# Kernel tuning notes

Hardware: AMD Instinct MI355X
Metric: run time of the kernel (lower is better)

Reference implementation:

```python
import jax, jax.numpy as jnp
import numpy as np
import math

H = 8
E = 512
D_K = E // H
NEG = -1000000000.0
# last (and only surviving) row of dist_bar: one threshold per head
DIST_BAR = np.array([0.2, 0.3, 0.4, 0.5, 0.6, 0.7, 0.8, 0.9], dtype=np.float32)


def setup_inputs() -> dict:
    key = jax.random.key(0)
    ks = jax.random.split(key, 12)
    B, N = 8, 1024
    s = 1.0 / math.sqrt(E)
    inp = {
        "query": jax.random.normal(ks[0], (B, N, E), jnp.float32),
        "key": jax.random.normal(ks[1], (B, N, E), jnp.float32),
        "value": jax.random.normal(ks[2], (B, N, E), jnp.float32),
        "dist": jax.random.uniform(ks[3], (B, 1, N, N), jnp.float32),
        "mask": jnp.ones((B, N, N), jnp.int32),
        "Wq": jax.random.normal(ks[4], (E, E), jnp.float32) * s,
        "bq": jnp.zeros((E,), jnp.float32),
        "Wk": jax.random.normal(ks[5], (E, E), jnp.float32) * s,
        "bk": jnp.zeros((E,), jnp.float32),
        "Wv": jax.random.normal(ks[6], (E, E), jnp.float32) * s,
        "bv": jnp.zeros((E,), jnp.float32),
        "Wo": jax.random.normal(ks[7], (E, E), jnp.float32) * s,
        "bo": jnp.zeros((E,), jnp.float32),
    }
    return inp


def reference(query, key, value, dist, mask, Wq, bq, Wk, bk, Wv, bv, Wo, bo):
    B, N, _ = query.shape
    # project and split heads: [B, H, N, D_K]
    def heads(x, W, b):
        return (x @ W.T + b).reshape(B, N, H, D_K).transpose(0, 2, 1, 3)
    q = heads(query, Wq, bq)
    k = heads(key, Wk, bk)
    v = heads(value, Wv, bv)
    scores = jnp.einsum("bhqd,bhkd->bhqk", q, k) / math.sqrt(D_K)
    # padding mask: [B,N,N] -> [B,1,N,N]
    scores = jnp.where(mask[:, None, :, :] == 0, NEG, scores)
    # per-head distance mask: dist [B,1,N,N] < thr[h] -> [B,H,N,N]
    thr = jnp.asarray(DIST_BAR)[None, :, None, None]
    dmask = dist < thr
    # first row/col (global atom) always attend
    dmask = dmask.at[:, :, 0, :].set(True).at[:, :, :, 0].set(True)
    scores = jnp.where(dmask, scores, NEG)
    p = jax.nn.softmax(scores, axis=-1)
    out = jnp.einsum("bhqk,bhkd->bhqd", p, v)  # [B,H,N,D_K]
    out = out.transpose(0, 2, 1, 3).reshape(B, N, H * D_K)
    return out @ Wo.T + bo
```

## Files before the change

### kernel.cpp

```cpp
#include <hip/hip_runtime.h>
#include <stdint.h>


typedef __attribute__((ext_vector_type(8))) short short8;
typedef __attribute__((ext_vector_type(4))) float floatx4;

#define MFMA16(a, b, c) __builtin_amdgcn_mfma_f32_16x16x32_bf16((a), (b), (c), 0, 0, 0)

static __device__ __forceinline__ unsigned short f2bf(float f) {
  union { float f; unsigned u; } v; v.f = f;
  unsigned r = v.u + 0x7fffu + ((v.u >> 16) & 1u);
  return (unsigned short)(r >> 16);
}

static __device__ __forceinline__ void gload_lds16(const void* g, void* l) {
  __builtin_amdgcn_global_load_lds((const __attribute__((address_space(1))) unsigned int*)g,
                                   (__attribute__((address_space(3))) unsigned int*)l,
                                   16, 0, 0);
}
static __device__ __forceinline__ int xsw(int row) { return (row & 3) ^ ((row >> 2) & 3); }

__global__ void wcast_kernel(const float* __restrict__ Wq, const float* __restrict__ Wk,
                             const float* __restrict__ Wv, const float* __restrict__ Wo,
                             unsigned short* __restrict__ o0, unsigned short* __restrict__ o1,
                             unsigned short* __restrict__ o2, unsigned short* __restrict__ o3) {
  int i = blockIdx.x * blockDim.x + threadIdx.x;
  int w = i >> 16, loc = i & 65535;
  const float* s = (w == 0) ? Wq : (w == 1) ? Wk : (w == 2) ? Wv : Wo;
  unsigned short* d = (w == 0) ? o0 : (w == 1) ? o1 : (w == 2) ? o2 : o3;
  float4 v = ((const float4*)s)[loc];
  ushort4 o;
  o.x = f2bf(v.x); o.y = f2bf(v.y); o.z = f2bf(v.z); o.w = f2bf(v.w);
  ((ushort4*)d)[loc] = o;
}

__global__ void codes_kernel(const float* __restrict__ dist, const int* __restrict__ mask,
                             unsigned char* __restrict__ codesP) {
  int t = blockIdx.x * blockDim.x + threadIdx.x;
  int flat = t << 2;
  int b = flat >> 20;
  int rem = flat & ((1 << 20) - 1);
  int row = rem >> 10;
  int col0 = rem & 1023;
  float4 d4 = ((const float4*)dist)[t];
  int4 m4 = ((const int4*)mask)[t];
  float dv[4] = {d4.x, d4.y, d4.z, d4.w};
  int mv[4] = {m4.x, m4.y, m4.z, m4.w};
  int rg = row >> 5;
  int st = (row >> 4) & 1;
  int qq = (row >> 2) & 3;
  int r = row & 3;
  size_t rowbase = (size_t)(b * 32 + rg) * 32768;
  int sub = st * 32 + r;
#pragma unroll
  for (int u = 0; u < 4; u++) {
    int col = col0 + u;
    float d = dv[u];
    int hmin = (d >= 0.2f) + (d >= 0.3f) + (d >= 0.4f) + (d >= 0.5f) +
               (d >= 0.6f) + (d >= 0.7f) + (d >= 0.8f) + (d >= 0.9f);
    unsigned char cc = (unsigned char)hmin;
    if (row == 0 || col == 0) cc = 0;
    if (mv[u] == 0) cc = 9;
    int kt = col >> 7, ci = (col >> 4) & 7, c = col & 15;
    int lane = qq * 16 + c;
    codesP[rowbase + (size_t)kt * 4096 + lane * 64 + sub + ci * 4] = cc;
  }
}

__global__ __launch_bounds__(256) void qkv_gemm(
    const float* __restrict__ Aq, const float* __restrict__ Ak, const float* __restrict__ Av,
    const unsigned short* __restrict__ Wqp, const unsigned short* __restrict__ Wkp,
    const unsigned short* __restrict__ Wvp,
    const float* __restrict__ bq, const float* __restrict__ bk, const float* __restrict__ bv,
    unsigned short* __restrict__ Qh, unsigned short* __restrict__ Kh,
    unsigned short* __restrict__ Vt) {
  const int z = blockIdx.z;
  const float* A = (z == 0) ? Aq : (z == 1) ? Ak : Av;
  const unsigned short* W = (z == 0) ? Wqp : (z == 1) ? Wkp : Wvp;
  const float* bias = (z == 0) ? bq : (z == 1) ? bk : bv;
  unsigned short* O = (z == 0) ? Qh : (z == 1) ? Kh : Vt;

  __shared__ __align__(16) short As[64 * 40];
  __shared__ __align__(16) short Bs[128 * 32];
  const int tid = threadIdx.x;
  const int lane = tid & 63;
  const int wave = tid >> 6;
  const int c = lane & 15;
  const int q = lane >> 4;
  const int m0 = blockIdx.x * 64;
  const int n0 = blockIdx.y * 128;
  const int wr = (wave >> 1) * 32;
  const int wc = (wave & 1) * 64;

  floatx4 acc[2][4];
#pragma unroll
  for (int i = 0; i < 2; i++)
#pragma unroll
    for (int j = 0; j < 4; j++) acc[i][j] = (floatx4)(0.0f);

  const int arow = tid >> 2, ach = tid & 3;
  const float* Ab = A + (size_t)(m0 + arow) * 512 + ach * 8;

  for (int k0 = 0; k0 < 512; k0 += 32) {
    __syncthreads();
#pragma unroll
    for (int it = 0; it < 2; it++) {
      int slot = wave * 128 + it * 64 + lane;
      int brow = slot >> 2, bch = slot & 3;
      int g = bch ^ xsw(brow);
      gload_lds16(W + (size_t)(n0 + brow) * 512 + k0 + g * 8,
                  &Bs[(size_t)(wave * 128 + it * 64) * 8]);
    }
    float4 a0 = *(const float4*)(Ab + k0);
    float4 a1 = *(const float4*)(Ab + k0 + 4);
    short8 av;
    av[0] = (short)f2bf(a0.x); av[1] = (short)f2bf(a0.y);
    av[2] = (short)f2bf(a0.z); av[3] = (short)f2bf(a0.w);
    av[4] = (short)f2bf(a1.x); av[5] = (short)f2bf(a1.y);
    av[6] = (short)f2bf(a1.z); av[7] = (short)f2bf(a1.w);
    *(short8*)(&As[arow * 40 + ach * 8]) = av;
    __syncthreads();

    short8 af[2], bfv[4];
#pragma unroll
    for (int i = 0; i < 2; i++)
      af[i] = *(const short8*)(&As[(wr + i * 16 + c) * 40 + q * 8]);
#pragma unroll
    for (int j = 0; j < 4; j++) {
      int row = wc + j * 16 + c;
      bfv[j] = *(const short8*)(&Bs[row * 32 + (q ^ xsw(row)) * 8]);
    }
#pragma unroll
    for (int i = 0; i < 2; i++)
#pragma unroll
      for (int j = 0; j < 4; j++)
        acc[i][j] = MFMA16(af[i], bfv[j], acc[i][j]);
  }

#pragma unroll
  for (int i = 0; i < 2; i++) {
    int gm0 = m0 + wr + i * 16 + q * 4;
#pragma unroll
    for (int j = 0; j < 4; j++) {
      int gn = n0 + wc + j * 16 + c;
      float bb = bias[gn];
      int h = gn >> 6, d = gn & 63;
      if (z == 2) {
        int b = gm0 >> 10, n = gm0 & 1023;
        ushort4 pk;
#pragma unroll
        for (int r = 0; r < 4; r++) pk[r] = f2bf(acc[i][j][r] + bb);
        *(ushort4*)(&Vt[(((size_t)(b * 8 + h) * 64 + d) << 10) + n]) = pk;
      } else {
#pragma unroll
        for (int r = 0; r < 4; r++) {
          int m = gm0 + r;
          int b = m >> 10, n = m & 1023;
          O[((((size_t)(b * 8 + h)) << 10) + n) * 64 + d] = f2bf(acc[i][j][r] + bb);
        }
      }
    }
  }
}

__global__ __launch_bounds__(256) void out_gemm(const unsigned short* __restrict__ A,
                                                const unsigned short* __restrict__ W,
                                                const float* __restrict__ bias,
                                                float* __restrict__ Out) {
  __shared__ __align__(16) short As[64 * 32];
  __shared__ __align__(16) short Bs[128 * 32];
  const int tid = threadIdx.x;
  const int lane = tid & 63;
  const int wave = tid >> 6;
  const int c = lane & 15;
  const int q = lane >> 4;
  const int m0 = blockIdx.x * 64;
  const int n0 = blockIdx.y * 128;
  const int wr = (wave >> 1) * 32;
  const int wc = (wave & 1) * 64;

  floatx4 acc[2][4];
#pragma unroll
  for (int i = 0; i < 2; i++)
#pragma unroll
    for (int j = 0; j < 4; j++) acc[i][j] = (floatx4)(0.0f);

  for (int k0 = 0; k0 < 512; k0 += 32) {
    __syncthreads();
    {
      int slot = wave * 64 + lane;
      int arow = slot >> 2, ach = slot & 3;
      int g = ach ^ xsw(arow);
      gload_lds16(A + (size_t)(m0 + arow) * 512 + k0 + g * 8, &As[(size_t)(wave * 64) * 8]);
    }
#pragma unroll
    for (int it = 0; it < 2; it++) {
      int slot = wave * 128 + it * 64 + lane;
      int brow = slot >> 2, bch = slot & 3;
      int g = bch ^ xsw(brow);
      gload_lds16(W + (size_t)(n0 + brow) * 512 + k0 + g * 8,
                  &Bs[(size_t)(wave * 128 + it * 64) * 8]);
    }
    __syncthreads();

    short8 af[2], bfv[4];
#pragma unroll
    for (int i = 0; i < 2; i++) {
      int row = wr + i * 16 + c;
      af[i] = *(const short8*)(&As[row * 32 + (q ^ xsw(row)) * 8]);
    }
#pragma unroll
    for (int j = 0; j < 4; j++) {
      int row = wc + j * 16 + c;
      bfv[j] = *(const short8*)(&Bs[row * 32 + (q ^ xsw(row)) * 8]);
    }
#pragma unroll
    for (int i = 0; i < 2; i++)
#pragma unroll
      for (int j = 0; j < 4; j++)
        acc[i][j] = MFMA16(af[i], bfv[j], acc[i][j]);
  }

#pragma unroll
  for (int i = 0; i < 2; i++) {
    int gm0 = m0 + wr + i * 16 + q * 4;
#pragma unroll
    for (int j = 0; j < 4; j++) {
      int gn = n0 + wc + j * 16 + c;
      float bb = bias[gn];
#pragma unroll
      for (int r = 0; r < 4; r++)
        Out[(size_t)(gm0 + r) * 512 + gn] = acc[i][j][r] + bb;
    }
  }
}

__global__ __launch_bounds__(256, 3) void attn_kernel(const unsigned short* __restrict__ Qh,
                                                      const unsigned short* __restrict__ Kh,
                                                      const unsigned short* __restrict__ Vt,
                                                      const unsigned char* __restrict__ codesP,
                                                      unsigned short* __restrict__ AO) {
  __shared__ __align__(16) unsigned short P[4][32 * 132];
  const int tid = threadIdx.x;
  const int lane = tid & 63;
  const int wave = tid >> 6;
  const int wsub = wave & 1;
  const int whalf = wave >> 1;
  const int c = lane & 15;
  const int q = lane >> 4;
  const int bh = blockIdx.y;
  const int b = bh >> 3;
  const int h = bh & 7;
  const size_t base = (size_t)bh << 16;
  const int rbase = blockIdx.x * 64 + wsub * 32;
  const int rg = rbase >> 5;
  unsigned short* Pw = &P[wave][0];

  short8 aq[2][2];
#pragma unroll
  for (int st = 0; st < 2; st++)
#pragma unroll
    for (int kk = 0; kk < 2; kk++)
      aq[st][kk] = *(const short8*)(Qh + base + (size_t)(rbase + st * 16 + c) * 64 + kk * 32 + q * 8);

  const unsigned char* cbt = codesP + (size_t)(b * 32 + rg) * 32768 + lane * 64;
  const unsigned short* Kb = Kh + base;
  const unsigned short* Vb = Vt + base;

  float rs[2][4];
#pragma unroll
  for (int st = 0; st < 2; st++)
#pragma unroll
    for (int r = 0; r < 4; r++) rs[st][r] = 0.0f;
  floatx4 o[2][4];
#pragma unroll
  for (int st = 0; st < 2; st++)
#pragma unroll
    for (int ci = 0; ci < 4; ci++) o[st][ci] = (floatx4)(0.0f);

  for (int kti = 0; kti < 4; kti++) {
    const int kt = whalf * 4 + kti;
    const unsigned short* Kt = Kb + (size_t)kt * 128 * 64;
    const unsigned char* cp = cbt + (size_t)kt * 4096;
#pragma unroll
    for (int j = 0; j < 4; j++) {
      floatx4 s[2][2];
      s[0][0] = (floatx4)(0.0f); s[0][1] = (floatx4)(0.0f);
      s[1][0] = (floatx4)(0.0f); s[1][1] = (floatx4)(0.0f);
#pragma unroll
      for (int u = 0; u < 2; u++) {
        int ci = 2 * j + u;
#pragma unroll
        for (int kk = 0; kk < 2; kk++) {
          short8 bk = *(const short8*)(Kt + (size_t)(ci * 16 + c) * 64 + kk * 32 + q * 8);
          s[0][u] = MFMA16(aq[0][kk], bk, s[0][u]);
          s[1][u] = MFMA16(aq[1][kk], bk, s[1][u]);
        }
      }
      uint2 cw0 = *(const uint2*)(cp + j * 8);
      uint2 cw1 = *(const uint2*)(cp + 32 + j * 8);
#pragma unroll
      for (int st = 0; st < 2; st++) {
        unsigned we = st ? cw1.x : cw0.x;
        unsigned wo = st ? cw1.y : cw0.y;
#pragma unroll
        for (int u = 0; u < 2; u++) {
          unsigned wv = u ? wo : we;
          int ci = 2 * j + u;
#pragma unroll
          for (int r = 0; r < 4; r++) {
            int code = (wv >> (r * 8)) & 0xff;
            float e = (h >= code) ? exp2f(s[st][u][r] * 0.1803368801111362f) : 0.0f;
            rs[st][r] += e;
            Pw[(st * 16 + q * 4 + r) * 132 + ci * 16 + c] = f2bf(e);
          }
        }
      }
      short8 ap0 = *(const short8*)(&Pw[(size_t)c * 132 + j * 32 + q * 8]);
      short8 ap1 = *(const short8*)(&Pw[(size_t)(16 + c) * 132 + j * 32 + q * 8]);
#pragma unroll
      for (int co = 0; co < 4; co++) {
        short8 bv = *(const short8*)(Vb + (size_t)(co * 16 + c) * 1024 + kt * 128 + j * 32 + q * 8);
        o[0][co] = MFMA16(ap0, bv, o[0][co]);
        o[1][co] = MFMA16(ap1, bv, o[1][co]);
      }
      __builtin_amdgcn_sched_barrier(0);
    }
  }

  float* Pf = (float*)&P[0][0];
  __syncthreads();
  if (whalf == 1) {
#pragma unroll
    for (int st = 0; st < 2; st++)
#pragma unroll
      for (int ci = 0; ci < 4; ci++)
        *(floatx4*)&Pf[(((wsub * 10 + st * 4 + ci) * 64) + lane) * 4] = o[st][ci];
#pragma unroll
    for (int st = 0; st < 2; st++) {
      floatx4 rr;
#pragma unroll
      for (int r = 0; r < 4; r++) rr[r] = rs[st][r];
      *(floatx4*)&Pf[(((wsub * 10 + 8 + st) * 64) + lane) * 4] = rr;
    }
  }
  __syncthreads();
  if (whalf == 1) return;

#pragma unroll
  for (int st = 0; st < 2; st++)
#pragma unroll
    for (int ci = 0; ci < 4; ci++) {
      floatx4 p = *(const floatx4*)&Pf[(((wsub * 10 + st * 4 + ci) * 64) + lane) * 4];
      o[st][ci] += p;
    }
#pragma unroll
  for (int st = 0; st < 2; st++) {
    floatx4 pr = *(const floatx4*)&Pf[(((wsub * 10 + 8 + st) * 64) + lane) * 4];
#pragma unroll
    for (int r = 0; r < 4; r++) rs[st][r] += pr[r];
  }

  float inv[2][4];
#pragma unroll
  for (int st = 0; st < 2; st++)
#pragma unroll
    for (int r = 0; r < 4; r++) {
      float v = rs[st][r];
      v += __shfl_xor(v, 1); v += __shfl_xor(v, 2);
      v += __shfl_xor(v, 4); v += __shfl_xor(v, 8);
      inv[st][r] = 1.0f / v;
    }
#pragma unroll
  for (int st = 0; st < 2; st++)
#pragma unroll
    for (int r = 0; r < 4; r++) {
      int n = rbase + st * 16 + q * 4 + r;
      size_t ob = ((size_t)((b << 10) + n)) * 512 + h * 64;
#pragma unroll
      for (int ci = 0; ci < 4; ci++)
        AO[ob + ci * 16 + c] = f2bf(o[st][ci][r] * inv[st][r]);
    }
}

extern "C" void kernel_launch(void* const* d_in, const int* in_sizes, int n_in,
                              void* d_out, int out_size, void* d_ws, size_t ws_size,
                              hipStream_t stream) {
  const float* query = (const float*)d_in[0];
  const float* key_  = (const float*)d_in[1];
  const float* value = (const float*)d_in[2];
  const float* dist  = (const float*)d_in[3];
  const int*   mask  = (const int*)d_in[4];
  const float* Wq = (const float*)d_in[5];
  const float* bq = (const float*)d_in[6];
  const float* Wk = (const float*)d_in[7];
  const float* bk = (const float*)d_in[8];
  const float* Wv = (const float*)d_in[9];
  const float* bv = (const float*)d_in[10];
  const float* Wo = (const float*)d_in[11];
  const float* bo = (const float*)d_in[12];

  char* ws = (char*)d_ws;
  size_t off = 0;
  auto alloc = [&](size_t bytes) -> char* {
    char* p = ws + off;
    off += (bytes + 255) & ~(size_t)255;
    return p;
  };
  const size_t NQKV = 8192ull * 512;
  unsigned short* wq16 = (unsigned short*)alloc(512ull * 512 * 2);
  unsigned short* wk16 = (unsigned short*)alloc(512ull * 512 * 2);
  unsigned short* wv16 = (unsigned short*)alloc(512ull * 512 * 2);
  unsigned short* wo16 = (unsigned short*)alloc(512ull * 512 * 2);
  unsigned short* Qh = (unsigned short*)alloc(NQKV * 2);
  unsigned short* Kh = (unsigned short*)alloc(NQKV * 2);
  unsigned short* Vt = (unsigned short*)alloc(NQKV * 2);
  unsigned short* AO = (unsigned short*)alloc(NQKV * 2);
  unsigned char*  codesP = (unsigned char*)alloc(8ull * 1024 * 1024);

  wcast_kernel<<<1024, 256, 0, stream>>>(Wq, Wk, Wv, Wo, wq16, wk16, wv16, wo16);
  codes_kernel<<<8192, 256, 0, stream>>>(dist, mask, codesP);
  qkv_gemm<<<dim3(128, 4, 3), 256, 0, stream>>>(query, key_, value, wq16, wk16, wv16,
                                                bq, bk, bv, Qh, Kh, Vt);
  attn_kernel<<<dim3(16, 64), 256, 0, stream>>>(Qh, Kh, Vt, codesP, AO);
  out_gemm<<<dim3(128, 4), 256, 0, stream>>>(AO, wo16, bo, (float*)d_out);
}
```

Baseline: 290.5 us.

## Transpose score MFMA so each lane owns a query row and packs P writes

Swaps the MFMA operand order so the score tile comes out transposed, with each lane holding four consecutive key columns of one query row. That lets P be converted with packed bf16 conversions and written to LDS as one 8-byte store, and collapses the row-sum bookkeeping into one scalar per sub-tile with a two-step cross-lane reduction. The codes kernel is re-laid out to match, writing four mask codes as one packed 32-bit store instead of four byte stores. The cost is an extra shuffle broadcast of the inverse sums in the epilogue and a layout coupling between the two kernels that must stay consistent.

Measured after the change: 283.0 us. 1.03x faster.

```diff
diff --git a/kernel.cpp b/kernel.cpp
--- a/kernel.cpp
+++ b/kernel.cpp
@@ -48,23 +48,26 @@
   int mv[4] = {m4.x, m4.y, m4.z, m4.w};
   int rg = row >> 5;
   int st = (row >> 4) & 1;
-  int qq = (row >> 2) & 3;
-  int r = row & 3;
+  int c = row & 15;
   size_t rowbase = (size_t)(b * 32 + rg) * 32768;
-  int sub = st * 32 + r;
+  int kt = col0 >> 7;
+  int colk = col0 & 127;
+  int ci = colk >> 4;
+  int hi = (colk >> 2) & 3;
+  int lane = hi * 16 + c;
+  unsigned pack = 0;
 #pragma unroll
   for (int u = 0; u < 4; u++) {
     int col = col0 + u;
     float d = dv[u];
     int hmin = (d >= 0.2f) + (d >= 0.3f) + (d >= 0.4f) + (d >= 0.5f) +
                (d >= 0.6f) + (d >= 0.7f) + (d >= 0.8f) + (d >= 0.9f);
-    unsigned char cc = (unsigned char)hmin;
+    unsigned cc = (unsigned)hmin;
     if (row == 0 || col == 0) cc = 0;
     if (mv[u] == 0) cc = 9;
-    int kt = col >> 7, ci = (col >> 4) & 7, c = col & 15;
-    int lane = qq * 16 + c;
-    codesP[rowbase + (size_t)kt * 4096 + lane * 64 + sub + ci * 4] = cc;
-  }
+    pack |= cc << (u * 8);
+  }
+  *(unsigned*)&codesP[rowbase + (size_t)kt * 4096 + lane * 64 + st * 32 + ci * 4] = pack;
 }
 
 __global__ __launch_bounds__(256) void qkv_gemm(
@@ -267,11 +270,7 @@
   const unsigned short* Kb = Kh + base;
   const unsigned short* Vb = Vt + base;
 
-  float rs[2][4];
-#pragma unroll
-  for (int st = 0; st < 2; st++)
-#pragma unroll
-    for (int r = 0; r < 4; r++) rs[st][r] = 0.0f;
+  float rsum[2] = {0.0f, 0.0f};
   floatx4 o[2][4];
 #pragma unroll
   for (int st = 0; st < 2; st++)
@@ -284,36 +283,39 @@
     const unsigned char* cp = cbt + (size_t)kt * 4096;
 #pragma unroll
     for (int j = 0; j < 4; j++) {
-      floatx4 s[2][2];
-      s[0][0] = (floatx4)(0.0f); s[0][1] = (floatx4)(0.0f);
-      s[1][0] = (floatx4)(0.0f); s[1][1] = (floatx4)(0.0f);
+      floatx4 s2[2][2];
+      s2[0][0] = (floatx4)(0.0f); s2[0][1] = (floatx4)(0.0f);
+      s2[1][0] = (floatx4)(0.0f); s2[1][1] = (floatx4)(0.0f);
 #pragma unroll
       for (int u = 0; u < 2; u++) {
         int ci = 2 * j + u;
 #pragma unroll
         for (int kk = 0; kk < 2; kk++) {
           short8 bk = *(const short8*)(Kt + (size_t)(ci * 16 + c) * 64 + kk * 32 + q * 8);
-          s[0][u] = MFMA16(aq[0][kk], bk, s[0][u]);
-          s[1][u] = MFMA16(aq[1][kk], bk, s[1][u]);
+          s2[0][u] = MFMA16(bk, aq[0][kk], s2[0][u]);
+          s2[1][u] = MFMA16(bk, aq[1][kk], s2[1][u]);
         }
       }
       uint2 cw0 = *(const uint2*)(cp + j * 8);
       uint2 cw1 = *(const uint2*)(cp + 32 + j * 8);
 #pragma unroll
       for (int st = 0; st < 2; st++) {
-        unsigned we = st ? cw1.x : cw0.x;
-        unsigned wo = st ? cw1.y : cw0.y;
 #pragma unroll
         for (int u = 0; u < 2; u++) {
-          unsigned wv = u ? wo : we;
-          int ci = 2 * j + u;
+          unsigned w = st ? (u ? cw1.y : cw1.x) : (u ? cw0.y : cw0.x);
+          float ev[4];
 #pragma unroll
           for (int r = 0; r < 4; r++) {
-            int code = (wv >> (r * 8)) & 0xff;
-            float e = (h >= code) ? exp2f(s[st][u][r] * 0.1803368801111362f) : 0.0f;
-            rs[st][r] += e;
-            Pw[(st * 16 + q * 4 + r) * 132 + ci * 16 + c] = f2bf(e);
+            int code = (w >> (r * 8)) & 0xff;
+            float ee = (h >= code) ? exp2f(s2[st][u][r] * 0.1803368801111362f) : 0.0f;
+            rsum[st] += ee;
+            ev[r] = ee;
           }
+          unsigned p0, p1;
+          asm("v_cvt_pk_bf16_f32 %0, %1, %2" : "=v"(p0) : "v"(ev[0]), "v"(ev[1]));
+          asm("v_cvt_pk_bf16_f32 %0, %1, %2" : "=v"(p1) : "v"(ev[2]), "v"(ev[3]));
+          uint2 pk; pk.x = p0; pk.y = p1;
+          *(uint2*)(&Pw[(st * 16 + c) * 132 + (2 * j + u) * 16 + q * 4]) = pk;
         }
       }
       short8 ap0 = *(const short8*)(&Pw[(size_t)c * 132 + j * 32 + q * 8]);
@@ -335,14 +337,9 @@
     for (int st = 0; st < 2; st++)
 #pragma unroll
       for (int ci = 0; ci < 4; ci++)
-        *(floatx4*)&Pf[(((wsub * 10 + st * 4 + ci) * 64) + lane) * 4] = o[st][ci];
-#pragma unroll
-    for (int st = 0; st < 2; st++) {
-      floatx4 rr;
-#pragma unroll
-      for (int r = 0; r < 4; r++) rr[r] = rs[st][r];
-      *(floatx4*)&Pf[(((wsub * 10 + 8 + st) * 64) + lane) * 4] = rr;
-    }
+        *(floatx4*)&Pf[(((wsub * 9 + st * 4 + ci) * 64) + lane) * 4] = o[st][ci];
+    float2 rr; rr.x = rsum[0]; rr.y = rsum[1];
+    *(float2*)&Pf[(((wsub * 9 + 8) * 64) + lane) * 4] = rr;
   }
   __syncthreads();
   if (whalf == 1) return;
@@ -351,26 +348,29 @@
   for (int st = 0; st < 2; st++)
 #pragma unroll
     for (int ci = 0; ci < 4; ci++) {
-      floatx4 p = *(const floatx4*)&Pf[(((wsub * 10 + st * 4 + ci) * 64) + lane) * 4];
+      floatx4 p = *(const floatx4*)&Pf[(((wsub * 9 + st * 4 + ci) * 64) + lane) * 4];
       o[st][ci] += p;
     }
+  {
+    float2 pr = *(const float2*)&Pf[(((wsub * 9 + 8) * 64) + lane) * 4];
+    rsum[0] += pr.x; rsum[1] += pr.y;
+  }
+
+  float inv2[2];
 #pragma unroll
   for (int st = 0; st < 2; st++) {
-    floatx4 pr = *(const floatx4*)&Pf[(((wsub * 10 + 8 + st) * 64) + lane) * 4];
-#pragma unroll
-    for (int r = 0; r < 4; r++) rs[st][r] += pr[r];
-  }
-
-  float inv[2][4];
+    float v = rsum[st];
+    v += __shfl_xor(v, 16);
+    v += __shfl_xor(v, 32);
+    inv2[st] = 1.0f / v;
+  }
+  const int sb = (lane & 48) + ((lane & 48) >> 2);
+  float iv[2][4];
 #pragma unroll
   for (int st = 0; st < 2; st++)
 #pragma unroll
-    for (int r = 0; r < 4; r++) {
-      float v = rs[st][r];
-      v += __shfl_xor(v, 1); v += __shfl_xor(v, 2);
-      v += __shfl_xor(v, 4); v += __shfl_xor(v, 8);
-      inv[st][r] = 1.0f / v;
-    }
+    for (int r = 0; r < 4; r++) iv[st][r] = __shfl(inv2[st], sb + r);
+
 #pragma unroll
   for (int st = 0; st < 2; st++)
 #pragma unroll
@@ -379,7 +379,7 @@
       size_t ob = ((size_t)((b << 10) + n)) * 512 + h * 64;
 #pragma unroll
       for (int ci = 0; ci < 4; ci++)
-        AO[ob + ci * 16 + c] = f2bf(o[st][ci][r] * inv[st][r]);
+        AO[ob + ci * 16 + c] = f2bf(o[st][ci][r] * iv[st][r]);
     }
 }
 
```
